# Performance work log

Hardware: AMD Instinct MI355X
Metric: run time of the kernel (lower is better)

## Reference

```python
import jax, jax.numpy as jnp
import numpy as np

PATCH_SIZE = 14.0
PIXEL_THRESHOLD = 5.0


def setup_inputs() -> dict:
    key = jax.random.key(0)
    k1, k2, k3, k4, k5 = jax.random.split(key, 5)
    B, N = 32, 1024
    src_pts = jax.random.uniform(k1, (B, N, 2), dtype=jnp.float32) * 32.0  # patch coords
    tar_pts = jax.random.uniform(k2, (B, N, 2), dtype=jnp.float32) * 32.0
    scores = jax.random.uniform(k3, (B, N), dtype=jnp.float32)
    relScale = 0.5 + jax.random.uniform(k4, (B, N), dtype=jnp.float32)  # positive scales
    theta = jax.random.uniform(k5, (B, N), dtype=jnp.float32) * 2.0 * np.pi
    relInplane = jnp.stack([jnp.cos(theta), jnp.sin(theta)], axis=-1)  # (B,N,2) cos,sin
    return {"src_pts": src_pts, "tar_pts": tar_pts, "scores": scores,
            "relScale": relScale, "relInplane": relInplane}


def _ransac_single(src, tar, score, scale, inplane):
    # src, tar: (N,2); score, scale: (N,); inplane: (N,2) = (cos, sin)
    N = src.shape[0]
    valid = src[:, 0] != -1.0  # (N,) sentinel mask from original forward
    s = src * PATCH_SIZE
    t = tar * PATCH_SIZE
    c, si = inplane[:, 0], inplane[:, 1]
    # R = [[c, -s], [s, c]] per candidate -> (N,2,2)
    R = jnp.stack([jnp.stack([c, -si], -1), jnp.stack([si, c], -1)], -2)
    A = scale[:, None, None] * R                          # (N,2,2) linear part
    trans = t - jnp.einsum('nij,nj->ni', A, s)            # (N,2) translation so A@s_n + t_n == t_n
    # candidate n applied to every point m (leave-one-out handled by masking diag)
    pred = jnp.einsum('nij,mj->nmi', A, s) + trans[:, None, :]   # (N,N,2)
    err = jnp.linalg.norm(pred - t[None, :, :], axis=-1)          # (N,N)
    not_self = ~jnp.eye(N, dtype=bool)
    inlier = (err <= PIXEL_THRESHOLD) & valid[None, :] & not_self  # (N,N)
    score_inl = jnp.sum(inlier * score[None, :], axis=1)           # (N,)
    score_inl = jnp.where(valid, score_inl, -1.0)
    best = jnp.argmax(score_inl)
    failed = score_inl[best] == 0.0
    M = (jnp.eye(3, dtype=src.dtype)
         .at[:2, :2].set(A[best])
         .at[:2, 2].set(trans[best]))
    # pack inliers of best candidate to the front (original index order preserved)
    inl = inlier[best]                                   # (N,) bool
    order = jnp.argsort(jnp.where(inl, 0, 1), stable=True)
    cnt = jnp.sum(inl)
    keep = jnp.arange(N) < cnt
    out_src = jnp.where(keep[:, None], src[order], -1.0)
    out_tar = jnp.where(keep[:, None], tar[order], -1.0)
    out_sc = jnp.where(keep, score[order], 0.0)
    return M, failed, out_src, out_tar, out_sc


def reference(src_pts, tar_pts, scores, relScale, relInplane):
    Ms, failed, inl_src, inl_tar, inl_sc = jax.vmap(_ransac_single)(
        src_pts, tar_pts, scores, relScale, relInplane)
    return Ms, failed, inl_src, inl_tar, inl_sc
```

## Files before the change

### kernel.cpp

```cpp
#include <hip/hip_runtime.h>

constexpr int BB = 32;
constexpr int NN = 1024;
constexpr int HYP = 128;
constexpr int HALF = 512;
constexpr int WAVES = 16;
constexpr int ITERS = HALF / WAVES;
#define PATCH 14.0f
#define THRSQ 25.0f

__global__ __launch_bounds__(1024, 8) void ransac_score_kernel(
    const float* __restrict__ src, const float* __restrict__ tar,
    const float* __restrict__ scores, const float* __restrict__ relScale,
    const float* __restrict__ relInplane, float* __restrict__ score_part)
{
#pragma clang fp contract(off)
    const int bid  = blockIdx.x;
    const int half = bid & 1;
    const int g    = (bid >> 1) & 7;
    const int b    = bid >> 4;
    const int tid  = threadIdx.x;
    const int wave = tid >> 6;
    const int lane = tid & 63;

    __shared__ float4 pts[HALF];
    __shared__ float  sc[HALF];
    __shared__ float  partial[WAVES][HYP];

    const float2* src2 = (const float2*)src + (size_t)b * NN;
    const float2* tar2 = (const float2*)tar + (size_t)b * NN;
    const float*  scb  = scores + (size_t)b * NN;
    const int mOff = half * HALF;

    if (tid < HALF) {
        float2 s = src2[mOff + tid];
        float2 t = tar2[mOff + tid];
        pts[tid] = make_float4(s.x * PATCH, s.y * PATCH, t.x * PATCH, t.y * PATCH);
        sc[tid]  = (s.x != -1.0f) ? scb[mOff + tid] : 0.0f;
    }

    const int n0 = g * HYP + lane;
    const int n1 = n0 + 64;
    const size_t nb = (size_t)b * NN;

    const float sv0 = relScale[nb + n0];
    const float sv1 = relScale[nb + n1];
    const float2 ip0 = ((const float2*)relInplane)[nb + n0];
    const float2 ip1 = ((const float2*)relInplane)[nb + n1];
    float2 s0 = src2[n0], t0 = tar2[n0];
    float2 s1 = src2[n1], t1 = tar2[n1];

    const float a00_0 = sv0 * ip0.x, a01_0 = sv0 * (-ip0.y);
    const float a10_0 = sv0 * ip0.y, a11_0 = sv0 * ip0.x;
    const float a00_1 = sv1 * ip1.x, a01_1 = sv1 * (-ip1.y);
    const float a10_1 = sv1 * ip1.y, a11_1 = sv1 * ip1.x;

    const float P0x = s0.x * PATCH, P0y = s0.y * PATCH;
    const float T0x = t0.x * PATCH, T0y = t0.y * PATCH;
    const float P1x = s1.x * PATCH, P1y = s1.y * PATCH;
    const float T1x = t1.x * PATCH, T1y = t1.y * PATCH;

    const float trx0 = T0x - (a00_0 * P0x + a01_0 * P0y);
    const float try0 = T0y - (a10_0 * P0x + a11_0 * P0y);
    const float trx1 = T1x - (a00_1 * P1x + a01_1 * P1y);
    const float try1 = T1y - (a10_1 * P1x + a11_1 * P1y);

    __syncthreads();

    float acc0 = 0.0f, acc1 = 0.0f;
    const int mBeg = wave * ITERS;
#pragma unroll 8
    for (int mm = 0; mm < ITERS; ++mm) {
        const float4 q = pts[mBeg + mm];
        const float  w = sc[mBeg + mm];

        float px0 = a00_0 * q.x + a01_0 * q.y + trx0;
        float py0 = a10_0 * q.x + a11_0 * q.y + try0;
        float dx0 = px0 - q.z, dy0 = py0 - q.w;
        float e20 = dx0 * dx0 + dy0 * dy0;
        acc0 += (e20 <= THRSQ) ? w : 0.0f;

        float px1 = a00_1 * q.x + a01_1 * q.y + trx1;
        float py1 = a10_1 * q.x + a11_1 * q.y + try1;
        float dx1 = px1 - q.z, dy1 = py1 - q.w;
        float e21 = dx1 * dx1 + dy1 * dy1;
        acc1 += (e21 <= THRSQ) ? w : 0.0f;
    }
    partial[wave][lane]      = acc0;
    partial[wave][lane + 64] = acc1;
    __syncthreads();

    if (tid < HYP) {
        float p = 0.0f;
#pragma unroll
        for (int w = 0; w < WAVES; ++w) p += partial[w][tid];
        const int n = g * HYP + tid;
        if ((g >> 2) == half) p -= sc[n - mOff];
        score_part[((size_t)half * BB + b) * NN + n] = p;
    }
}

__global__ __launch_bounds__(1024) void ransac_select_kernel(
    const float* __restrict__ src, const float* __restrict__ tar,
    const float* __restrict__ scores, const float* __restrict__ relScale,
    const float* __restrict__ relInplane,
    const float* __restrict__ score_part, float* __restrict__ out)
{
#pragma clang fp contract(off)
    const int b = blockIdx.x;
    const int tid = threadIdx.x;
    const int lane = tid & 63;
    const int wave = tid >> 6;

    __shared__ float wvalSh[16];
    __shared__ int   widxSh[16];
    __shared__ float prm[6];
    __shared__ int   bestIdxSh;
    __shared__ float bestValSh;
    __shared__ int   wcnt[16], wbase[16];
    __shared__ float osx[NN], osy[NN], otx[NN], oty[NN], osc[NN];

    const size_t gm = (size_t)b * NN + tid;
    const float2 s2 = ((const float2*)src)[gm];
    const float2 t2 = ((const float2*)tar)[gm];
    const float scin = scores[gm];

    float val;
    {
        float p = score_part[(size_t)b * NN + tid]
                + score_part[((size_t)BB + b) * NN + tid];
        val = (s2.x != -1.0f) ? p : -1.0f;
    }
    int idx = tid;

    for (int d = 1; d < 64; d <<= 1) {
        float ov = __shfl_xor(val, d);
        int   oi = __shfl_xor(idx, d);
        if (ov > val || (ov == val && oi < idx)) { val = ov; idx = oi; }
    }
    if (lane == 0) { wvalSh[wave] = val; widxSh[wave] = idx; }
    __syncthreads();
    if (tid < 64) {
        float v = (tid < 16) ? wvalSh[tid] : -1e30f;
        int   i = (tid < 16) ? widxSh[tid] : 0x7fffffff;
        for (int d = 1; d < 16; d <<= 1) {
            float ov = __shfl_xor(v, d);
            int   oi = __shfl_xor(i, d);
            if (ov > v || (ov == v && oi < i)) { v = ov; i = oi; }
        }
        if (tid == 0) { bestIdxSh = i; bestValSh = v; }
    }
    __syncthreads();
    const int best = bestIdxSh;

    if (tid == 0) {
        size_t gi = (size_t)b * NN + best;
        float scale = relScale[gi];
        float c  = relInplane[gi * 2];
        float si = relInplane[gi * 2 + 1];
        float a00 = scale * c;
        float a01 = scale * (-si);
        float a10 = scale * si;
        float a11 = scale * c;
        float snx = src[gi * 2] * PATCH, sny = src[gi * 2 + 1] * PATCH;
        float tnx = tar[gi * 2] * PATCH, tny = tar[gi * 2 + 1] * PATCH;
        float trx = tnx - (a00 * snx + a01 * sny);
        float trY = tny - (a10 * snx + a11 * sny);
        prm[0] = a00; prm[1] = a01; prm[2] = a10; prm[3] = a11; prm[4] = trx; prm[5] = trY;

        float* M = out + (size_t)b * 9;
        M[0] = a00; M[1] = a01; M[2] = trx;
        M[3] = a10; M[4] = a11; M[5] = trY;
        M[6] = 0.0f; M[7] = 0.0f; M[8] = 1.0f;
        out[(size_t)BB * 9 + b] = (bestValSh == 0.0f) ? 1.0f : 0.0f;
    }
    __syncthreads();

    float sx = s2.x * PATCH, sy = s2.y * PATCH;
    float tx = t2.x * PATCH, ty = t2.y * PATCH;
    float px = prm[0] * sx + prm[1] * sy + prm[4];
    float py = prm[2] * sx + prm[3] * sy + prm[5];
    float dx = px - tx, dy = py - ty;
    bool flag = (dx * dx + dy * dy <= THRSQ) && (s2.x != -1.0f) && (tid != best);

    unsigned long long mask = __ballot(flag);
    int posInWave = __popcll(mask & ((1ULL << lane) - 1ULL));
    if (lane == 0) wcnt[wave] = __popcll(mask);
    __syncthreads();
    if (tid < 16) {
        int s = 0;
        for (int i = 0; i < tid; ++i) s += wcnt[i];
        wbase[tid] = s;
    }
    __syncthreads();
    int pos = wbase[wave] + posInWave;

    osx[tid] = -1.0f; osy[tid] = -1.0f;
    otx[tid] = -1.0f; oty[tid] = -1.0f;
    osc[tid] = 0.0f;
    __syncthreads();
    if (flag) {
        osx[pos] = s2.x; osy[pos] = s2.y;
        otx[pos] = t2.x; oty[pos] = t2.y;
        osc[pos] = scin;
    }
    __syncthreads();

    const size_t O_SRC = (size_t)BB * 9 + BB;
    const size_t O_TAR = O_SRC + (size_t)BB * NN * 2;
    const size_t O_SC  = O_TAR + (size_t)BB * NN * 2;
    out[O_SRC + gm * 2]     = osx[tid];
    out[O_SRC + gm * 2 + 1] = osy[tid];
    out[O_TAR + gm * 2]     = otx[tid];
    out[O_TAR + gm * 2 + 1] = oty[tid];
    out[O_SC  + gm]         = osc[tid];
}

extern "C" void kernel_launch(void* const* d_in, const int* in_sizes, int n_in,
                              void* d_out, int out_size, void* d_ws, size_t ws_size,
                              hipStream_t stream) {
    const float* src        = (const float*)d_in[0];
    const float* tar        = (const float*)d_in[1];
    const float* scores     = (const float*)d_in[2];
    const float* relScale   = (const float*)d_in[3];
    const float* relInplane = (const float*)d_in[4];
    float* out = (float*)d_out;
    float* score_part = (float*)d_ws;

    ransac_score_kernel<<<BB * 8 * 2, 1024, 0, stream>>>(
        src, tar, scores, relScale, relInplane, score_part);
    ransac_select_kernel<<<BB, NN, 0, stream>>>(
        src, tar, scores, relScale, relInplane, score_part, out);
}
```

Measured before the change: 21.75 us.

## Retile scoring kernel to 4 hypotheses per thread over point quarters

The scoring kernel now uses 512-thread blocks. Each thread evaluates 4 hypotheses against a quarter of the points, where before it evaluated 2 hypotheses against half. The result is 4 partial score buffers, and the select kernel sums them. This raises register-level reuse of each shared-memory point load and halves the threads launched, at the cost of an extra partial-sum read and higher register pressure.

After: 21.28 us. 2.1% less time.

```diff
diff --git a/kernel.cpp b/kernel.cpp
--- a/kernel.cpp
+++ b/kernel.cpp
@@ -2,101 +2,87 @@
 
 constexpr int BB = 32;
 constexpr int NN = 1024;
-constexpr int HYP = 128;
-constexpr int HALF = 512;
-constexpr int WAVES = 16;
-constexpr int ITERS = HALF / WAVES;
+constexpr int TPB = 512;
+constexpr int WAVES = 8;
+constexpr int GH = 256;
+constexpr int MQ = 256;
+constexpr int ITERS = MQ / WAVES;
 #define PATCH 14.0f
 #define THRSQ 25.0f
 
-__global__ __launch_bounds__(1024, 8) void ransac_score_kernel(
+__global__ __launch_bounds__(TPB, 3) void ransac_score_kernel(
     const float* __restrict__ src, const float* __restrict__ tar,
     const float* __restrict__ scores, const float* __restrict__ relScale,
     const float* __restrict__ relInplane, float* __restrict__ score_part)
 {
 #pragma clang fp contract(off)
     const int bid  = blockIdx.x;
-    const int half = bid & 1;
-    const int g    = (bid >> 1) & 7;
+    const int q    = bid & 3;
+    const int g    = (bid >> 2) & 3;
     const int b    = bid >> 4;
     const int tid  = threadIdx.x;
     const int wave = tid >> 6;
     const int lane = tid & 63;
 
-    __shared__ float4 pts[HALF];
-    __shared__ float  sc[HALF];
-    __shared__ float  partial[WAVES][HYP];
+    __shared__ float4 pts[MQ];
+    __shared__ float  sc[MQ];
+    __shared__ float  partial[WAVES][GH];
 
     const float2* src2 = (const float2*)src + (size_t)b * NN;
     const float2* tar2 = (const float2*)tar + (size_t)b * NN;
     const float*  scb  = scores + (size_t)b * NN;
-    const int mOff = half * HALF;
-
-    if (tid < HALF) {
+    const int mOff = q * MQ;
+
+    if (tid < MQ) {
         float2 s = src2[mOff + tid];
         float2 t = tar2[mOff + tid];
         pts[tid] = make_float4(s.x * PATCH, s.y * PATCH, t.x * PATCH, t.y * PATCH);
         sc[tid]  = (s.x != -1.0f) ? scb[mOff + tid] : 0.0f;
     }
 
-    const int n0 = g * HYP + lane;
-    const int n1 = n0 + 64;
     const size_t nb = (size_t)b * NN;
-
-    const float sv0 = relScale[nb + n0];
-    const float sv1 = relScale[nb + n1];
-    const float2 ip0 = ((const float2*)relInplane)[nb + n0];
-    const float2 ip1 = ((const float2*)relInplane)[nb + n1];
-    float2 s0 = src2[n0], t0 = tar2[n0];
-    float2 s1 = src2[n1], t1 = tar2[n1];
-
-    const float a00_0 = sv0 * ip0.x, a01_0 = sv0 * (-ip0.y);
-    const float a10_0 = sv0 * ip0.y, a11_0 = sv0 * ip0.x;
-    const float a00_1 = sv1 * ip1.x, a01_1 = sv1 * (-ip1.y);
-    const float a10_1 = sv1 * ip1.y, a11_1 = sv1 * ip1.x;
-
-    const float P0x = s0.x * PATCH, P0y = s0.y * PATCH;
-    const float T0x = t0.x * PATCH, T0y = t0.y * PATCH;
-    const float P1x = s1.x * PATCH, P1y = s1.y * PATCH;
-    const float T1x = t1.x * PATCH, T1y = t1.y * PATCH;
-
-    const float trx0 = T0x - (a00_0 * P0x + a01_0 * P0y);
-    const float try0 = T0y - (a10_0 * P0x + a11_0 * P0y);
-    const float trx1 = T1x - (a00_1 * P1x + a01_1 * P1y);
-    const float try1 = T1y - (a10_1 * P1x + a11_1 * P1y);
-
-    __syncthreads();
-
-    float acc0 = 0.0f, acc1 = 0.0f;
+    float a00[4], a01[4], a10[4], a11[4], trx[4], trY[4];
+#pragma unroll
+    for (int h = 0; h < 4; ++h) {
+        const int n = g * GH + h * 64 + lane;
+        const float sv  = relScale[nb + n];
+        const float2 ip = ((const float2*)relInplane)[nb + n];
+        float2 s = src2[n], t = tar2[n];
+        a00[h] = sv * ip.x;  a01[h] = sv * (-ip.y);
+        a10[h] = sv * ip.y;  a11[h] = sv * ip.x;
+        const float Px = s.x * PATCH, Py = s.y * PATCH;
+        const float Tx = t.x * PATCH, Ty = t.y * PATCH;
+        trx[h] = Tx - (a00[h] * Px + a01[h] * Py);
+        trY[h] = Ty - (a10[h] * Px + a11[h] * Py);
+    }
+
+    __syncthreads();
+
+    float acc[4] = {0.0f, 0.0f, 0.0f, 0.0f};
     const int mBeg = wave * ITERS;
-#pragma unroll 8
+#pragma unroll 4
     for (int mm = 0; mm < ITERS; ++mm) {
-        const float4 q = pts[mBeg + mm];
-        const float  w = sc[mBeg + mm];
-
-        float px0 = a00_0 * q.x + a01_0 * q.y + trx0;
-        float py0 = a10_0 * q.x + a11_0 * q.y + try0;
-        float dx0 = px0 - q.z, dy0 = py0 - q.w;
-        float e20 = dx0 * dx0 + dy0 * dy0;
-        acc0 += (e20 <= THRSQ) ? w : 0.0f;
-
-        float px1 = a00_1 * q.x + a01_1 * q.y + trx1;
-        float py1 = a10_1 * q.x + a11_1 * q.y + try1;
-        float dx1 = px1 - q.z, dy1 = py1 - q.w;
-        float e21 = dx1 * dx1 + dy1 * dy1;
-        acc1 += (e21 <= THRSQ) ? w : 0.0f;
-    }
-    partial[wave][lane]      = acc0;
-    partial[wave][lane + 64] = acc1;
-    __syncthreads();
-
-    if (tid < HYP) {
+        const float4 qp = pts[mBeg + mm];
+        const float  w  = sc[mBeg + mm];
+#pragma unroll
+        for (int h = 0; h < 4; ++h) {
+            float px = a00[h] * qp.x + a01[h] * qp.y + trx[h];
+            float py = a10[h] * qp.x + a11[h] * qp.y + trY[h];
+            float dx = px - qp.z, dy = py - qp.w;
+            float e2 = dx * dx + dy * dy;
+            acc[h] += (e2 <= THRSQ) ? w : 0.0f;
+        }
+    }
+#pragma unroll
+    for (int h = 0; h < 4; ++h) partial[wave][h * 64 + lane] = acc[h];
+    __syncthreads();
+
+    if (tid < GH) {
         float p = 0.0f;
 #pragma unroll
         for (int w = 0; w < WAVES; ++w) p += partial[w][tid];
-        const int n = g * HYP + tid;
-        if ((g >> 2) == half) p -= sc[n - mOff];
-        score_part[((size_t)half * BB + b) * NN + n] = p;
+        if (g == q) p -= sc[tid];
+        score_part[((size_t)q * BB + b) * NN + g * GH + tid] = p;
     }
 }
 
@@ -128,7 +114,9 @@
     float val;
     {
         float p = score_part[(size_t)b * NN + tid]
-                + score_part[((size_t)BB + b) * NN + tid];
+                + score_part[((size_t)BB + b) * NN + tid]
+                + score_part[((size_t)2 * BB + b) * NN + tid]
+                + score_part[((size_t)3 * BB + b) * NN + tid];
         val = (s2.x != -1.0f) ? p : -1.0f;
     }
     int idx = tid;
@@ -227,7 +215,7 @@
     float* out = (float*)d_out;
     float* score_part = (float*)d_ws;
 
-    ransac_score_kernel<<<BB * 8 * 2, 1024, 0, stream>>>(
+    ransac_score_kernel<<<BB * 4 * 4, TPB, 0, stream>>>(
         src, tar, scores, relScale, relInplane, score_part);
     ransac_select_kernel<<<BB, NN, 0, stream>>>(
         src, tar, scores, relScale, relInplane, score_part, out);
```
